# Performance work log

Hardware: AMD Instinct MI355X
Metric: run time of the kernel (lower is better)

Reference implementation:

```python
import jax, jax.numpy as jnp
import numpy as np
from jax.ops import segment_sum

N_NODES = 50000
N_EDGES = 800000
D_IN, D_HID, D_OUT = 128, 128, 64


def setup_inputs() -> dict:
    key = jax.random.key(0)
    ks = jax.random.split(key, 7)
    return {
        "src": jax.random.randint(ks[0], (N_EDGES,), 0, N_NODES, dtype=jnp.int32),
        "dst": jax.random.randint(ks[1], (N_EDGES,), 0, N_NODES, dtype=jnp.int32),
        "x": jax.random.normal(ks[2], (N_NODES, D_IN), dtype=jnp.float32),
        "W1": jax.random.normal(ks[3], (D_IN, D_HID), dtype=jnp.float32) * (1.0 / np.sqrt(D_IN)),
        "b1": jnp.zeros((D_HID,), dtype=jnp.float32),
        "W2": jax.random.normal(ks[4], (D_HID, D_OUT), dtype=jnp.float32) * (1.0 / np.sqrt(D_HID)),
        "b2": jnp.zeros((D_OUT,), dtype=jnp.float32),
    }


def _gcn_layer(src, dst, x, W, b, inv_sqrt_out, inv_sqrt_in):
    # DGL GraphConv, norm='both': h = D_in^{-1/2} A D_out^{-1/2} (x W) + b
    h = (x * inv_sqrt_out[:, None]) @ W          # transform first (in >= out)
    msg = h[src]                                  # gather source messages [E, d]
    agg = segment_sum(msg, dst, num_segments=x.shape[0])
    return agg * inv_sqrt_in[:, None] + b


def reference(src, dst, x, W1, b1, W2, b2):
    n = x.shape[0]
    ones = jnp.ones((src.shape[0],), dtype=x.dtype)
    deg_out = jnp.clip(segment_sum(ones, src, num_segments=n), 1.0)
    deg_in = jnp.clip(segment_sum(ones, dst, num_segments=n), 1.0)
    inv_sqrt_out = jax.lax.rsqrt(deg_out)
    inv_sqrt_in = jax.lax.rsqrt(deg_in)
    h = _gcn_layer(src, dst, x, W1, b1, inv_sqrt_out, inv_sqrt_in)
    h = jax.nn.relu(h)
    h = _gcn_layer(src, dst, h, W2, b2, inv_sqrt_out, inv_sqrt_in)
    return h
```

## Files before the change

kernel.cpp:

```cpp
#include <hip/hip_runtime.h>
#include <hip/hip_fp16.h>

#define D_IN  128
#define D_HID 128
#define D_OUT 64
#define NBMAX 512
#define CHUNK 2048
#define FCACHE 3072

typedef __attribute__((ext_vector_type(8))) short bf16x8;
typedef __attribute__((ext_vector_type(4))) float f32x4;

__device__ __forceinline__ unsigned short f2bf_rne(float f) {
    unsigned int u = __float_as_uint(f);
    return (unsigned short)((u + 0x7FFFu + ((u >> 16) & 1u)) >> 16);
}

__launch_bounds__(256)
__global__ void k_prep(const float* __restrict__ W1, const float* __restrict__ W2,
                       unsigned short* __restrict__ W1h, unsigned short* __restrict__ W1l,
                       unsigned short* __restrict__ W2h, unsigned short* __restrict__ W2l,
                       int* __restrict__ cntD, int* __restrict__ cntS, int NB) {
    const int b = blockIdx.x, t = threadIdx.x;
    if (b < 64) {
        const int i = b * 256 + t;
        const int k = i >> 7, j = i & 127;
        const float v = W1[i];
        const unsigned short hb = f2bf_rne(v);
        const float hf = __uint_as_float((unsigned int)hb << 16);
        W1h[j * 128 + k] = hb;
        W1l[j * 128 + k] = f2bf_rne(v - hf);
    } else if (b < 96) {
        const int i = (b - 64) * 256 + t;
        const int k = i >> 6, j = i & 63;
        const float v = W2[i];
        const unsigned short hb = f2bf_rne(v);
        const float hf = __uint_as_float((unsigned int)hb << 16);
        W2h[j * 128 + k] = hb;
        W2l[j * 128 + k] = f2bf_rne(v - hf);
    } else {
        for (int i = t; i < NB; i += 256) { cntD[i] = 0; cntS[i] = 0; }
    }
}

struct BucketS {
    int lc[512], ls[512];
    int baD[512], baS[512];
    int gbD[512], gbS[512];
    int ssum[256];
    unsigned int  ldsD[CHUNK];
    int           gposD[CHUNK];
    unsigned char ldsS[CHUNK];
    int           gposS[CHUNK];
};
struct GemmS {
    short Ah[32][136];
    short Al[32][136];
};
union SMem { BucketS b; GemmS g; };

__device__ __forceinline__ void bucket_body(
        BucketS& sm, int bx,
        const int* __restrict__ src, const int* __restrict__ dst,
        int E, int NB, int cap,
        int* __restrict__ cntD, int* __restrict__ cntS,
        unsigned int* __restrict__ storeD, unsigned char* __restrict__ storeS) {
    const int t = threadIdx.x;
    const int e0 = bx * CHUNK;
    const int e1 = min(e0 + CHUNK, E);
    const int n  = e1 - e0;

    int sv[8], dv[8];
#pragma unroll
    for (int u = 0; u < 8; ++u) {
        const int i = e0 + u * 256 + t;
        if (i < e1) { sv[u] = src[i]; dv[u] = dst[i]; }
        else        { sv[u] = -1;     dv[u] = -1; }
    }

    sm.lc[t] = 0; sm.lc[t + 256] = 0; sm.ls[t] = 0; sm.ls[t + 256] = 0;
    __syncthreads();
#pragma unroll
    for (int u = 0; u < 8; ++u) {
        if (sv[u] >= 0) {
            atomicAdd(&sm.lc[dv[u] >> 7], 1);
            atomicAdd(&sm.ls[sv[u] >> 7], 1);
        }
    }
    __syncthreads();

    const int c0 = sm.lc[2 * t], c1 = sm.lc[2 * t + 1];
    const int s0 = sm.ls[2 * t], s1 = sm.ls[2 * t + 1];
    {
        const int pc = c0 + c1;
        sm.ssum[t] = pc; __syncthreads();
        int inc = pc;
        for (int off = 1; off < 256; off <<= 1) {
            const int o = (t >= off) ? sm.ssum[t - off] : 0;
            __syncthreads();
            inc += o; sm.ssum[t] = inc;
            __syncthreads();
        }
        const int ex = inc - pc;
        sm.baD[2 * t] = ex; sm.baD[2 * t + 1] = ex + c0;
    }
    {
        const int ps = s0 + s1;
        sm.ssum[t] = ps; __syncthreads();
        int inc = ps;
        for (int off = 1; off < 256; off <<= 1) {
            const int o = (t >= off) ? sm.ssum[t - off] : 0;
            __syncthreads();
            inc += o; sm.ssum[t] = inc;
            __syncthreads();
        }
        const int ex = inc - ps;
        sm.baS[2 * t] = ex; sm.baS[2 * t + 1] = ex + s0;
    }
    __syncthreads();

    for (int i = t; i < NB; i += 256) {
        const int c = sm.lc[i];
        sm.gbD[i] = i * cap + (c ? atomicAdd(&cntD[i], c) : 0);
        const int s = sm.ls[i];
        sm.gbS[i] = i * cap + (s ? atomicAdd(&cntS[i], s) : 0);
    }
    __syncthreads();
    sm.lc[t] = 0; sm.lc[t + 256] = 0; sm.ls[t] = 0; sm.ls[t + 256] = 0;
    __syncthreads();

#pragma unroll
    for (int u = 0; u < 8; ++u) {
        if (sv[u] >= 0) {
            const int s = sv[u], d = dv[u];
            const int bd = d >> 7;
            const int lp = atomicAdd(&sm.lc[bd], 1);
            const int p  = sm.baD[bd] + lp;
            sm.ldsD[p]  = (unsigned int)s | ((unsigned int)(d & 127) << 16);
            sm.gposD[p] = sm.gbD[bd] + lp;
            const int bs = s >> 7;
            const int lq = atomicAdd(&sm.ls[bs], 1);
            const int q  = sm.baS[bs] + lq;
            sm.ldsS[q]  = (unsigned char)(s & 127);
            sm.gposS[q] = sm.gbS[bs] + lq;
        }
    }
    __syncthreads();

    for (int p = t; p < n; p += 256) {
        storeD[sm.gposD[p]] = sm.ldsD[p];
        storeS[sm.gposS[p]] = sm.ldsS[p];
    }
}

__device__ __forceinline__ void gemm1_body(
        GemmS& sm, int bx,
        const float* __restrict__ X,
        const unsigned short* __restrict__ Wth, const unsigned short* __restrict__ Wtl,
        __half* __restrict__ Y, int N) {
    const int t = threadIdx.x;
    const int row0 = bx * 32;

#pragma unroll
    for (int p = 0; p < 4; ++p) {
        const int idx = p * 256 + t;
        const int r   = idx >> 5;
        const int c4  = (idx & 31) << 2;
        const int gr  = row0 + r;
        float4 v = make_float4(0.f, 0.f, 0.f, 0.f);
        if (gr < N) v = *(const float4*)(X + (long long)gr * 128 + c4);
        const float f[4] = {v.x, v.y, v.z, v.w};
        short hh[4], ll[4];
#pragma unroll
        for (int i = 0; i < 4; ++i) {
            const unsigned short hb = f2bf_rne(f[i]);
            const float hf = __uint_as_float(((unsigned int)hb) << 16);
            hh[i] = (short)hb;
            ll[i] = (short)f2bf_rne(f[i] - hf);
        }
        *(short4*)&sm.Ah[r][c4] = make_short4(hh[0], hh[1], hh[2], hh[3]);
        *(short4*)&sm.Al[r][c4] = make_short4(ll[0], ll[1], ll[2], ll[3]);
    }
    __syncthreads();

    constexpr int NT = 4;
    const int w    = t >> 6;
    const int lane = t & 63;
    const int rg = w & 1, cg = w >> 1;
    const int lrow = lane & 15;
    const int lk   = (lane >> 4) << 3;
    const int colbase = cg * (16 * NT);

    f32x4 acc[NT];
#pragma unroll
    for (int n = 0; n < NT; ++n) acc[n] = (f32x4){0.f, 0.f, 0.f, 0.f};

#pragma unroll
    for (int ks = 0; ks < 4; ++ks) {
        const int k = ks * 32 + lk;
        const bf16x8 ah = *(const bf16x8*)&sm.Ah[rg * 16 + lrow][k];
        const bf16x8 al = *(const bf16x8*)&sm.Al[rg * 16 + lrow][k];
#pragma unroll
        for (int n = 0; n < NT; ++n) {
            const int col = colbase + n * 16 + lrow;
            const bf16x8 bh = *(const bf16x8*)(Wth + (size_t)col * 128 + k);
            const bf16x8 bl = *(const bf16x8*)(Wtl + (size_t)col * 128 + k);
            acc[n] = __builtin_amdgcn_mfma_f32_16x16x32_bf16(ah, bh, acc[n], 0, 0, 0);
            acc[n] = __builtin_amdgcn_mfma_f32_16x16x32_bf16(ah, bl, acc[n], 0, 0, 0);
            acc[n] = __builtin_amdgcn_mfma_f32_16x16x32_bf16(al, bh, acc[n], 0, 0, 0);
        }
    }

#pragma unroll
    for (int n = 0; n < NT; ++n) {
#pragma unroll
        for (int i = 0; i < 4; ++i) {
            const int r = row0 + rg * 16 + ((lane >> 4) << 2) + i;
            if (r < N)
                Y[(long long)r * D_HID + colbase + n * 16 + lrow] = __float2half(acc[n][i]);
        }
    }
}

__launch_bounds__(256)
__global__ void k_bucket_gemm(const int* __restrict__ src, const int* __restrict__ dst,
                              int E, int NB, int cap,
                              int* __restrict__ cntD, int* __restrict__ cntS,
                              unsigned int* __restrict__ storeD, unsigned char* __restrict__ storeS,
                              const float* __restrict__ X,
                              const unsigned short* __restrict__ Wth,
                              const unsigned short* __restrict__ Wtl,
                              __half* __restrict__ Y, int N, int nbBlk) {
    __shared__ SMem sm;
    const int bx = (int)blockIdx.x;
    if (bx < nbBlk)
        bucket_body(sm.b, bx, src, dst, E, NB, cap, cntD, cntS, storeD, storeS);
    else
        gemm1_body(sm.g, bx - nbBlk, X, Wth, Wtl, Y, N);
}

__launch_bounds__(256)
__global__ void k_fin(const unsigned int* __restrict__ storeD, const unsigned char* __restrict__ storeS,
                      const int* __restrict__ cntD, const int* __restrict__ cntS,
                      int cap, int N, int NB, int E,
                      int* __restrict__ rowptr, float* __restrict__ inv_in,
                      float* __restrict__ inv_out, unsigned short* __restrict__ csr_src) {
    __shared__ int fh[128];
    __shared__ int sc[128];
    __shared__ int cur[128];
    __shared__ int red[256];
    __shared__ unsigned int ecache[FCACHE];
    const int b = blockIdx.x, t = threadIdx.x;
    const long long sb = (long long)b * cap;

    int partial = 0;
    for (int i = t; i < b; i += 256) partial += cntD[i];
    red[t] = partial;
    __syncthreads();
    for (int off = 128; off > 0; off >>= 1) {
        if (t < off) red[t] += red[t + off];
        __syncthreads();
    }
    const int base = red[0];

    const int cnt = cntD[b];
    const bool cached = (cnt <= FCACHE);
    if (cached) {
        for (int i = t; i < cnt; i += 256) ecache[i] = storeD[sb + i];
    }

    if (t < 128) fh[t] = 0;
    __syncthreads();
    for (int i = t; i < cnt; i += 256) {
        const unsigned int e = cached ? ecache[i] : storeD[sb + i];
        atomicAdd(&fh[e >> 16], 1);
    }
    __syncthreads();
    if (t < 128) sc[t] = fh[t];
    __syncthreads();
    int inc = (t < 128) ? sc[t] : 0;
    for (int off = 1; off < 128; off <<= 1) {
        int o = (t >= off && t < 128) ? sc[t - off] : 0;
        __syncthreads();
        if (t < 128) { inc += o; sc[t] = inc; }
        __syncthreads();
    }
    if (t < 128) {
        const int excl = inc - fh[t];
        cur[t] = excl;
        const int node = (b << 7) + t;
        if (node < N) {
            rowptr[node] = base + excl;
            inv_in[node] = rsqrtf((float)max(fh[t], 1));
        }
    }
    if (b == NB - 1 && t == 128) rowptr[N] = E;
    __syncthreads();
    for (int i = t; i < cnt; i += 256) {
        const unsigned int e = cached ? ecache[i] : storeD[sb + i];
        const int pos = atomicAdd(&cur[e >> 16], 1);
        csr_src[base + pos] = (unsigned short)(e & 0xFFFFu);
    }

    __syncthreads();
    if (t < 128) fh[t] = 0;
    __syncthreads();
    const int cnts = cntS[b];
    for (int i = t; i < cnts; i += 256) atomicAdd(&fh[storeS[sb + i]], 1);
    __syncthreads();
    if (t < 128) {
        const int node = (b << 7) + t;
        if (node < N) inv_out[node] = rsqrtf((float)max(fh[t], 1));
    }
}

template<int LDN>
__launch_bounds__(256)
__global__ void k_gemm_mfma(const __half* __restrict__ X,
                            const unsigned short* __restrict__ Wth,
                            const unsigned short* __restrict__ Wtl,
                            __half* __restrict__ Y, int N) {
    __shared__ short Ah[32][136], Al[32][136];

    const int t = threadIdx.x;
    const int row0 = blockIdx.x * 32;

#pragma unroll
    for (int p = 0; p < 2; ++p) {
        const int idx = p * 256 + t;
        const int r   = idx >> 4;
        const int c8  = (idx & 15) << 3;
        const int gr  = row0 + r;
        uint4 raw = make_uint4(0u, 0u, 0u, 0u);
        if (gr < N) raw = *(const uint4*)(X + (long long)gr * 128 + c8);
        const __half2* hp = (const __half2*)&raw;
        short hh[8], ll[8];
#pragma unroll
        for (int u = 0; u < 4; ++u) {
            const float2 f2 = __half22float2(hp[u]);
            const float f[2] = {f2.x, f2.y};
#pragma unroll
            for (int q = 0; q < 2; ++q) {
                const unsigned short hb = f2bf_rne(f[q]);
                const float hf = __uint_as_float(((unsigned int)hb) << 16);
                hh[2 * u + q] = (short)hb;
                ll[2 * u + q] = (short)f2bf_rne(f[q] - hf);
            }
        }
        *(short4*)&Ah[r][c8]     = make_short4(hh[0], hh[1], hh[2], hh[3]);
        *(short4*)&Ah[r][c8 + 4] = make_short4(hh[4], hh[5], hh[6], hh[7]);
        *(short4*)&Al[r][c8]     = make_short4(ll[0], ll[1], ll[2], ll[3]);
        *(short4*)&Al[r][c8 + 4] = make_short4(ll[4], ll[5], ll[6], ll[7]);
    }
    __syncthreads();

    constexpr int NT = LDN / 32;
    const int w    = t >> 6;
    const int lane = t & 63;
    const int rg = w & 1, cg = w >> 1;
    const int lrow = lane & 15;
    const int lk   = (lane >> 4) << 3;
    const int colbase = cg * (16 * NT);

    f32x4 acc[NT];
#pragma unroll
    for (int n = 0; n < NT; ++n) acc[n] = (f32x4){0.f, 0.f, 0.f, 0.f};

#pragma unroll
    for (int ks = 0; ks < 4; ++ks) {
        const int k = ks * 32 + lk;
        const bf16x8 ah = *(const bf16x8*)&Ah[rg * 16 + lrow][k];
        const bf16x8 al = *(const bf16x8*)&Al[rg * 16 + lrow][k];
#pragma unroll
        for (int n = 0; n < NT; ++n) {
            const int col = colbase + n * 16 + lrow;
            const bf16x8 bh = *(const bf16x8*)(Wth + (size_t)col * 128 + k);
            const bf16x8 bl = *(const bf16x8*)(Wtl + (size_t)col * 128 + k);
            acc[n] = __builtin_amdgcn_mfma_f32_16x16x32_bf16(ah, bh, acc[n], 0, 0, 0);
            acc[n] = __builtin_amdgcn_mfma_f32_16x16x32_bf16(ah, bl, acc[n], 0, 0, 0);
            acc[n] = __builtin_amdgcn_mfma_f32_16x16x32_bf16(al, bh, acc[n], 0, 0, 0);
        }
    }

#pragma unroll
    for (int n = 0; n < NT; ++n) {
#pragma unroll
        for (int i = 0; i < 4; ++i) {
            const int r = row0 + rg * 16 + ((lane >> 4) << 2) + i;
            if (r < N)
                Y[(long long)r * LDN + colbase + n * 16 + lrow] = __float2half(acc[n][i]);
        }
    }
}

template<int D, bool RELU, bool SRCSCALE, typename TO>
__launch_bounds__(256)
__global__ void k_gather(const int* __restrict__ rowptr, const unsigned short* __restrict__ csr_src,
                         const __half* __restrict__ Y, const float* __restrict__ inv_in,
                         const float* __restrict__ inv_out, const float* __restrict__ b,
                         TO* __restrict__ out, int N, const float* __restrict__ inv_src) {
    const int wid  = (int)((blockIdx.x * 256u + threadIdx.x) >> 6);
    const int lane = threadIdx.x & 63;
    if (wid >= N) return;

    const int start = rowptr[wid];
    const int end   = rowptr[wid + 1];

    constexpr int LPE = D / 8;
    constexpr int EPW = 64 / LPE;
    const int grp  = lane / LPE;
    const int colh = (lane % LPE) * 8;

    float a[8];
#pragma unroll
    for (int u = 0; u < 8; ++u) a[u] = 0.0f;

    auto accum = [&](uint4 raw, float io) {
        const __half2* h = (const __half2*)&raw;
#pragma unroll
        for (int u = 0; u < 4; ++u) {
            const float2 f = __half22float2(h[u]);
            if constexpr (SRCSCALE) {
                a[2 * u]     += f.x * io;
                a[2 * u + 1] += f.y * io;
            } else {
                a[2 * u]     += f.x;
                a[2 * u + 1] += f.y;
            }
        }
    };

    for (int k = start; k < end; k += 64) {
        const int idx = k + lane;
        const int sv  = (idx < end) ? (int)csr_src[idx] : 0;
        const int cnt = min(64, end - k);
        int j = 0;
        for (; j + 8 * EPW <= cnt; j += 8 * EPW) {
            int s[8];
#pragma unroll
            for (int u = 0; u < 8; ++u) s[u] = __shfl(sv, j + u * EPW + grp);
            uint4 r[8];
#pragma unroll
            for (int u = 0; u < 8; ++u) r[u] = *(const uint4*)(Y + (long long)s[u] * D + colh);
            float io[8];
            if constexpr (SRCSCALE) {
#pragma unroll
                for (int u = 0; u < 8; ++u) io[u] = inv_src[s[u]];
            }
#pragma unroll
            for (int u = 0; u < 8; ++u) accum(r[u], SRCSCALE ? io[u] : 0.0f);
        }
        for (; j + 4 * EPW <= cnt; j += 4 * EPW) {
            int s[4];
#pragma unroll
            for (int u = 0; u < 4; ++u) s[u] = __shfl(sv, j + u * EPW + grp);
            uint4 r[4];
#pragma unroll
            for (int u = 0; u < 4; ++u) r[u] = *(const uint4*)(Y + (long long)s[u] * D + colh);
            float io[4];
            if constexpr (SRCSCALE) {
#pragma unroll
                for (int u = 0; u < 4; ++u) io[u] = inv_src[s[u]];
            }
#pragma unroll
            for (int u = 0; u < 4; ++u) accum(r[u], SRCSCALE ? io[u] : 0.0f);
        }
        for (; j < cnt; j += EPW) {
            const int jj = j + grp;
            const int s  = __shfl(sv, jj);
            if (jj < cnt) {
                const uint4 r = *(const uint4*)(Y + (long long)s * D + colh);
                accum(r, SRCSCALE ? inv_src[s] : 0.0f);
            }
        }
    }

#pragma unroll
    for (int u = 0; u < 8; ++u) a[u] += __shfl_down(a[u], 32);
#pragma unroll
    for (int u = 0; u < 8; ++u) a[u] += __shfl_down(a[u], 16);
    if (EPW == 8) {
#pragma unroll
        for (int u = 0; u < 8; ++u) a[u] += __shfl_down(a[u], 8);
    }

    if (lane < LPE) {
        const float ii = inv_in[wid];
        const float io = RELU ? inv_out[wid] : 0.0f;
        const float4 b0 = *(const float4*)(b + colh);
        const float4 b1 = *(const float4*)(b + colh + 4);
        float r[8];
        r[0] = a[0] * ii + b0.x; r[1] = a[1] * ii + b0.y;
        r[2] = a[2] * ii + b0.z; r[3] = a[3] * ii + b0.w;
        r[4] = a[4] * ii + b1.x; r[5] = a[5] * ii + b1.y;
        r[6] = a[6] * ii + b1.z; r[7] = a[7] * ii + b1.w;
        if (RELU) {
#pragma unroll
            for (int u = 0; u < 8; ++u) r[u] = fmaxf(r[u], 0.0f) * io;
        }
        if constexpr (sizeof(TO) == 2) {
            __half2 h0 = __float22half2_rn(make_float2(r[0], r[1]));
            __half2 h1 = __float22half2_rn(make_float2(r[2], r[3]));
            __half2 h2 = __float22half2_rn(make_float2(r[4], r[5]));
            __half2 h3 = __float22half2_rn(make_float2(r[6], r[7]));
            uint4 pk;
            pk.x = *(unsigned int*)&h0; pk.y = *(unsigned int*)&h1;
            pk.z = *(unsigned int*)&h2; pk.w = *(unsigned int*)&h3;
            *(uint4*)((__half*)out + (long long)wid * D + colh) = pk;
        } else {
            float* o = (float*)out + (long long)wid * D + colh;
            *(float4*)(o)     = make_float4(r[0], r[1], r[2], r[3]);
            *(float4*)(o + 4) = make_float4(r[4], r[5], r[6], r[7]);
        }
    }
}

extern "C" void kernel_launch(void* const* d_in, const int* in_sizes, int n_in,
                              void* d_out, int out_size, void* d_ws, size_t ws_size,
                              hipStream_t stream) {
    const int*   src = (const int*)d_in[0];
    const int*   dst = (const int*)d_in[1];
    const float* x   = (const float*)d_in[2];
    const float* W1  = (const float*)d_in[3];
    const float* b1  = (const float*)d_in[4];
    const float* W2  = (const float*)d_in[5];
    const float* b2  = (const float*)d_in[6];
    float* out = (float*)d_out;

    const int E  = in_sizes[0];
    const int N  = in_sizes[2] / D_IN;
    const int NB = (N + 127) >> 7;
    const int mean = E / NB;
    const int cap  = mean + mean / 4 + 128;

    char* ws = (char*)d_ws;
    size_t off = 0;
    auto alloc = [&](size_t bytes) -> void* {
        void* p = ws + off;
        off += (bytes + 255) & ~(size_t)255;
        return p;
    };
    float*          inv_out = (float*)alloc((size_t)N * 4);
    float*          inv_in  = (float*)alloc((size_t)N * 4);
    int*            rowptr  = (int*)alloc((size_t)(N + 1) * 4);
    int*            cntD    = (int*)alloc((size_t)NB * 4);
    int*            cntS    = (int*)alloc((size_t)NB * 4);
    unsigned int*   storeD  = (unsigned int*)alloc((size_t)NB * cap * 4);
    unsigned char*  storeS  = (unsigned char*)alloc((size_t)NB * cap);
    unsigned short* csr_src = (unsigned short*)alloc((size_t)E * 2);
    unsigned short* W1h     = (unsigned short*)alloc(128 * 128 * 2);
    unsigned short* W1l     = (unsigned short*)alloc(128 * 128 * 2);
    unsigned short* W2h     = (unsigned short*)alloc(64 * 128 * 2);
    unsigned short* W2l     = (unsigned short*)alloc(64 * 128 * 2);
    __half*         Y1      = (__half*)alloc((size_t)N * D_HID * 2);
    __half*         H       = (__half*)alloc((size_t)N * D_HID * 2);
    __half*         Y2      = (__half*)alloc((size_t)N * D_OUT * 2);
    (void)ws_size; (void)n_in; (void)out_size;

    const int nbBlk   = (E + CHUNK - 1) / CHUNK;
    const int gemmBlk = (N + 31) / 32;

    k_prep<<<97, 256, 0, stream>>>(W1, W2, W1h, W1l, W2h, W2l, cntD, cntS, NB);
    k_bucket_gemm<<<nbBlk + gemmBlk, 256, 0, stream>>>(src, dst, E, NB, cap, cntD, cntS,
                                                       storeD, storeS, x, W1h, W1l, Y1, N, nbBlk);
    k_fin<<<NB, 256, 0, stream>>>(storeD, storeS, cntD, cntS, cap, N, NB, E,
                                  rowptr, inv_in, inv_out, csr_src);

    k_gather<D_HID, true, true, __half><<<(N + 3) / 4, 256, 0, stream>>>(
        rowptr, csr_src, Y1, inv_in, inv_out, b1, H, N, inv_out);

    k_gemm_mfma<D_OUT><<<(N + 31) / 32, 256, 0, stream>>>(H, W2h, W2l, Y2, N);
    k_gather<D_OUT, false, false, float><<<(N + 3) / 4, 256, 0, stream>>>(
        rowptr, csr_src, Y2, inv_in, nullptr, b2, out, N, nullptr);
}
```

Measured before the change: 134.1 us.

## Fuse layer-1 gather with layer-2 GEMM and use wave-shuffle scan in bucketing

Merges the first-layer neighbour aggregation (with ReLU and scaling) into the second-layer MFMA GEMM kernel. Each block now gathers 32 rows into shared memory as split bf16 and multiplies them straight away, so the fp16 intermediate H no longer goes through global memory and one launch disappears. The block-wide Hillis-Steele scan in the bucketing step becomes a wave-level shuffle scan plus a small cross-wave sum, which removes many barriers. In exchange, the fused gather runs with far fewer blocks, 8 rows per wave processed serially, and a shallower unroll, which reduces memory-level parallelism in the gather.

After: 141.3 us. 5.4% more time.

```diff
diff --git a/kernel.cpp b/kernel.cpp
--- a/kernel.cpp
+++ b/kernel.cpp
@@ -47,7 +47,7 @@
     int lc[512], ls[512];
     int baD[512], baS[512];
     int gbD[512], gbS[512];
-    int ssum[256];
+    int wsumD[4], wsumS[4];
     unsigned int  ldsD[CHUNK];
     int           gposD[CHUNK];
     unsigned char ldsS[CHUNK];
@@ -91,32 +91,26 @@
 
     const int c0 = sm.lc[2 * t], c1 = sm.lc[2 * t + 1];
     const int s0 = sm.ls[2 * t], s1 = sm.ls[2 * t + 1];
-    {
-        const int pc = c0 + c1;
-        sm.ssum[t] = pc; __syncthreads();
-        int inc = pc;
-        for (int off = 1; off < 256; off <<= 1) {
-            const int o = (t >= off) ? sm.ssum[t - off] : 0;
-            __syncthreads();
-            inc += o; sm.ssum[t] = inc;
-            __syncthreads();
-        }
-        const int ex = inc - pc;
-        sm.baD[2 * t] = ex; sm.baD[2 * t + 1] = ex + c0;
-    }
-    {
-        const int ps = s0 + s1;
-        sm.ssum[t] = ps; __syncthreads();
-        int inc = ps;
-        for (int off = 1; off < 256; off <<= 1) {
-            const int o = (t >= off) ? sm.ssum[t - off] : 0;
-            __syncthreads();
-            inc += o; sm.ssum[t] = inc;
-            __syncthreads();
-        }
-        const int ex = inc - ps;
-        sm.baS[2 * t] = ex; sm.baS[2 * t + 1] = ex + s0;
-    }
+    const int pc = c0 + c1, ps = s0 + s1;
+    const int wl = t & 63, wv = t >> 6;
+    int incD = pc, incS = ps;
+#pragma unroll
+    for (int off = 1; off < 64; off <<= 1) {
+        const int oD = __shfl_up(incD, off);
+        const int oS = __shfl_up(incS, off);
+        if (wl >= off) { incD += oD; incS += oS; }
+    }
+    if (wl == 63) { sm.wsumD[wv] = incD; sm.wsumS[wv] = incS; }
+    __syncthreads();
+    int baseD = 0, baseS = 0;
+#pragma unroll
+    for (int ww = 0; ww < 4; ++ww) {
+        if (ww < wv) { baseD += sm.wsumD[ww]; baseS += sm.wsumS[ww]; }
+    }
+    const int exD = baseD + incD - pc;
+    const int exS = baseS + incS - ps;
+    sm.baD[2 * t] = exD; sm.baD[2 * t + 1] = exD + c0;
+    sm.baS[2 * t] = exS; sm.baS[2 * t + 1] = exS + s0;
     __syncthreads();
 
     for (int i = t; i < NB; i += 256) {
@@ -314,53 +308,119 @@
     }
 }
 
-template<int LDN>
 __launch_bounds__(256)
-__global__ void k_gemm_mfma(const __half* __restrict__ X,
-                            const unsigned short* __restrict__ Wth,
-                            const unsigned short* __restrict__ Wtl,
-                            __half* __restrict__ Y, int N) {
+__global__ void k_gather_gemm2(const int* __restrict__ rowptr, const unsigned short* __restrict__ csr_src,
+                               const __half* __restrict__ Y1, const float* __restrict__ inv_in,
+                               const float* __restrict__ inv_out, const float* __restrict__ b1,
+                               const unsigned short* __restrict__ W2h, const unsigned short* __restrict__ W2l,
+                               __half* __restrict__ Y2, int N) {
     __shared__ short Ah[32][136], Al[32][136];
-
     const int t = threadIdx.x;
+    const int w = t >> 6, lane = t & 63;
     const int row0 = blockIdx.x * 32;
-
-#pragma unroll
-    for (int p = 0; p < 2; ++p) {
-        const int idx = p * 256 + t;
-        const int r   = idx >> 4;
-        const int c8  = (idx & 15) << 3;
-        const int gr  = row0 + r;
-        uint4 raw = make_uint4(0u, 0u, 0u, 0u);
-        if (gr < N) raw = *(const uint4*)(X + (long long)gr * 128 + c8);
-        const __half2* hp = (const __half2*)&raw;
-        short hh[8], ll[8];
-#pragma unroll
-        for (int u = 0; u < 4; ++u) {
-            const float2 f2 = __half22float2(hp[u]);
-            const float f[2] = {f2.x, f2.y};
-#pragma unroll
-            for (int q = 0; q < 2; ++q) {
-                const unsigned short hb = f2bf_rne(f[q]);
+    const int grp  = lane >> 4;
+    const int colh = (lane & 15) * 8;
+
+    for (int i = 0; i < 8; ++i) {
+        const int noderow = w * 8 + i;
+        const int wid = row0 + noderow;
+
+        float a[8];
+#pragma unroll
+        for (int u = 0; u < 8; ++u) a[u] = 0.0f;
+
+        if (wid < N) {
+            const int start = rowptr[wid];
+            const int end   = rowptr[wid + 1];
+            for (int k = start; k < end; k += 64) {
+                const int idx = k + lane;
+                const int svv = (idx < end) ? (int)csr_src[idx] : 0;
+                const int cnt = min(64, end - k);
+                int j = 0;
+                for (; j + 16 <= cnt; j += 16) {
+                    int s[4];
+#pragma unroll
+                    for (int u = 0; u < 4; ++u) s[u] = __shfl(svv, j + u * 4 + grp);
+                    uint4 r[4];
+#pragma unroll
+                    for (int u = 0; u < 4; ++u) r[u] = *(const uint4*)(Y1 + (long long)s[u] * 128 + colh);
+                    float io[4];
+#pragma unroll
+                    for (int u = 0; u < 4; ++u) io[u] = inv_out[s[u]];
+#pragma unroll
+                    for (int u = 0; u < 4; ++u) {
+                        const __half2* h = (const __half2*)&r[u];
+#pragma unroll
+                        for (int q = 0; q < 4; ++q) {
+                            const float2 f = __half22float2(h[q]);
+                            a[2 * q]     += f.x * io[u];
+                            a[2 * q + 1] += f.y * io[u];
+                        }
+                    }
+                }
+                for (; j < cnt; j += 4) {
+                    const int jj = j + grp;
+                    const int s  = __shfl(svv, jj);
+                    if (jj < cnt) {
+                        const uint4 r = *(const uint4*)(Y1 + (long long)s * 128 + colh);
+                        const float io = inv_out[s];
+                        const __half2* h = (const __half2*)&r;
+#pragma unroll
+                        for (int q = 0; q < 4; ++q) {
+                            const float2 f = __half22float2(h[q]);
+                            a[2 * q]     += f.x * io;
+                            a[2 * q + 1] += f.y * io;
+                        }
+                    }
+                }
+            }
+        }
+
+#pragma unroll
+        for (int u = 0; u < 8; ++u) a[u] += __shfl_down(a[u], 32);
+#pragma unroll
+        for (int u = 0; u < 8; ++u) a[u] += __shfl_down(a[u], 16);
+
+        if (lane < 16) {
+            float r[8];
+            if (wid < N) {
+                const float ii = inv_in[wid];
+                const float io = inv_out[wid];
+                const float4 b0v = *(const float4*)(b1 + colh);
+                const float4 b1v = *(const float4*)(b1 + colh + 4);
+                r[0] = fmaxf(a[0] * ii + b0v.x, 0.f) * io;
+                r[1] = fmaxf(a[1] * ii + b0v.y, 0.f) * io;
+                r[2] = fmaxf(a[2] * ii + b0v.z, 0.f) * io;
+                r[3] = fmaxf(a[3] * ii + b0v.w, 0.f) * io;
+                r[4] = fmaxf(a[4] * ii + b1v.x, 0.f) * io;
+                r[5] = fmaxf(a[5] * ii + b1v.y, 0.f) * io;
+                r[6] = fmaxf(a[6] * ii + b1v.z, 0.f) * io;
+                r[7] = fmaxf(a[7] * ii + b1v.w, 0.f) * io;
+            } else {
+#pragma unroll
+                for (int u = 0; u < 8; ++u) r[u] = 0.0f;
+            }
+            short hh[8], ll[8];
+#pragma unroll
+            for (int u = 0; u < 8; ++u) {
+                const unsigned short hb = f2bf_rne(r[u]);
                 const float hf = __uint_as_float(((unsigned int)hb) << 16);
-                hh[2 * u + q] = (short)hb;
-                ll[2 * u + q] = (short)f2bf_rne(f[q] - hf);
+                hh[u] = (short)hb;
+                ll[u] = (short)f2bf_rne(r[u] - hf);
             }
-        }
-        *(short4*)&Ah[r][c8]     = make_short4(hh[0], hh[1], hh[2], hh[3]);
-        *(short4*)&Ah[r][c8 + 4] = make_short4(hh[4], hh[5], hh[6], hh[7]);
-        *(short4*)&Al[r][c8]     = make_short4(ll[0], ll[1], ll[2], ll[3]);
-        *(short4*)&Al[r][c8 + 4] = make_short4(ll[4], ll[5], ll[6], ll[7]);
-    }
-    __syncthreads();
-
-    constexpr int NT = LDN / 32;
-    const int w    = t >> 6;
-    const int lane = t & 63;
+            *(short4*)&Ah[noderow][colh]     = make_short4(hh[0], hh[1], hh[2], hh[3]);
+            *(short4*)&Ah[noderow][colh + 4] = make_short4(hh[4], hh[5], hh[6], hh[7]);
+            *(short4*)&Al[noderow][colh]     = make_short4(ll[0], ll[1], ll[2], ll[3]);
+            *(short4*)&Al[noderow][colh + 4] = make_short4(ll[4], ll[5], ll[6], ll[7]);
+        }
+    }
+    __syncthreads();
+
+    constexpr int NT = 2;
     const int rg = w & 1, cg = w >> 1;
     const int lrow = lane & 15;
     const int lk   = (lane >> 4) << 3;
-    const int colbase = cg * (16 * NT);
+    const int colbase = cg * 32;
 
     f32x4 acc[NT];
 #pragma unroll
@@ -374,8 +434,8 @@
 #pragma unroll
         for (int n = 0; n < NT; ++n) {
             const int col = colbase + n * 16 + lrow;
-            const bf16x8 bh = *(const bf16x8*)(Wth + (size_t)col * 128 + k);
-            const bf16x8 bl = *(const bf16x8*)(Wtl + (size_t)col * 128 + k);
+            const bf16x8 bh = *(const bf16x8*)(W2h + (size_t)col * 128 + k);
+            const bf16x8 bl = *(const bf16x8*)(W2l + (size_t)col * 128 + k);
             acc[n] = __builtin_amdgcn_mfma_f32_16x16x32_bf16(ah, bh, acc[n], 0, 0, 0);
             acc[n] = __builtin_amdgcn_mfma_f32_16x16x32_bf16(ah, bl, acc[n], 0, 0, 0);
             acc[n] = __builtin_amdgcn_mfma_f32_16x16x32_bf16(al, bh, acc[n], 0, 0, 0);
@@ -388,17 +448,16 @@
         for (int i = 0; i < 4; ++i) {
             const int r = row0 + rg * 16 + ((lane >> 4) << 2) + i;
             if (r < N)
-                Y[(long long)r * LDN + colbase + n * 16 + lrow] = __float2half(acc[n][i]);
-        }
-    }
-}
-
-template<int D, bool RELU, bool SRCSCALE, typename TO>
+                Y2[(long long)r * D_OUT + colbase + n * 16 + lrow] = __float2half(acc[n][i]);
+        }
+    }
+}
+
+template<int D>
 __launch_bounds__(256)
 __global__ void k_gather(const int* __restrict__ rowptr, const unsigned short* __restrict__ csr_src,
                          const __half* __restrict__ Y, const float* __restrict__ inv_in,
-                         const float* __restrict__ inv_out, const float* __restrict__ b,
-                         TO* __restrict__ out, int N, const float* __restrict__ inv_src) {
+                         const float* __restrict__ b, float* __restrict__ out, int N) {
     const int wid  = (int)((blockIdx.x * 256u + threadIdx.x) >> 6);
     const int lane = threadIdx.x & 63;
     if (wid >= N) return;
@@ -415,18 +474,13 @@
 #pragma unroll
     for (int u = 0; u < 8; ++u) a[u] = 0.0f;
 
-    auto accum = [&](uint4 raw, float io) {
+    auto accum = [&](uint4 raw) {
         const __half2* h = (const __half2*)&raw;
 #pragma unroll
         for (int u = 0; u < 4; ++u) {
             const float2 f = __half22float2(h[u]);
-            if constexpr (SRCSCALE) {
-                a[2 * u]     += f.x * io;
-                a[2 * u + 1] += f.y * io;
-            } else {
-                a[2 * u]     += f.x;
-                a[2 * u + 1] += f.y;
-            }
+            a[2 * u]     += f.x;
+            a[2 * u + 1] += f.y;
         }
     };
 
@@ -442,13 +496,8 @@
             uint4 r[8];
 #pragma unroll
             for (int u = 0; u < 8; ++u) r[u] = *(const uint4*)(Y + (long long)s[u] * D + colh);
-            float io[8];
-            if constexpr (SRCSCALE) {
-#pragma unroll
-                for (int u = 0; u < 8; ++u) io[u] = inv_src[s[u]];
-            }
-#pragma unroll
-            for (int u = 0; u < 8; ++u) accum(r[u], SRCSCALE ? io[u] : 0.0f);
+#pragma unroll
+            for (int u = 0; u < 8; ++u) accum(r[u]);
         }
         for (; j + 4 * EPW <= cnt; j += 4 * EPW) {
             int s[4];
@@ -457,20 +506,15 @@
             uint4 r[4];
 #pragma unroll
             for (int u = 0; u < 4; ++u) r[u] = *(const uint4*)(Y + (long long)s[u] * D + colh);
-            float io[4];
-            if constexpr (SRCSCALE) {
-#pragma unroll
-                for (int u = 0; u < 4; ++u) io[u] = inv_src[s[u]];
-            }
-#pragma unroll
-            for (int u = 0; u < 4; ++u) accum(r[u], SRCSCALE ? io[u] : 0.0f);
+#pragma unroll
+            for (int u = 0; u < 4; ++u) accum(r[u]);
         }
         for (; j < cnt; j += EPW) {
             const int jj = j + grp;
             const int s  = __shfl(sv, jj);
             if (jj < cnt) {
                 const uint4 r = *(const uint4*)(Y + (long long)s * D + colh);
-                accum(r, SRCSCALE ? inv_src[s] : 0.0f);
+                accum(r);
             }
         }
     }
@@ -479,39 +523,18 @@
     for (int u = 0; u < 8; ++u) a[u] += __shfl_down(a[u], 32);
 #pragma unroll
     for (int u = 0; u < 8; ++u) a[u] += __shfl_down(a[u], 16);
-    if (EPW == 8) {
-#pragma unroll
-        for (int u = 0; u < 8; ++u) a[u] += __shfl_down(a[u], 8);
-    }
+#pragma unroll
+    for (int u = 0; u < 8; ++u) a[u] += __shfl_down(a[u], 8);
 
     if (lane < LPE) {
         const float ii = inv_in[wid];
-        const float io = RELU ? inv_out[wid] : 0.0f;
         const float4 b0 = *(const float4*)(b + colh);
         const float4 b1 = *(const float4*)(b + colh + 4);
-        float r[8];
-        r[0] = a[0] * ii + b0.x; r[1] = a[1] * ii + b0.y;
-        r[2] = a[2] * ii + b0.z; r[3] = a[3] * ii + b0.w;
-        r[4] = a[4] * ii + b1.x; r[5] = a[5] * ii + b1.y;
-        r[6] = a[6] * ii + b1.z; r[7] = a[7] * ii + b1.w;
-        if (RELU) {
-#pragma unroll
-            for (int u = 0; u < 8; ++u) r[u] = fmaxf(r[u], 0.0f) * io;
-        }
-        if constexpr (sizeof(TO) == 2) {
-            __half2 h0 = __float22half2_rn(make_float2(r[0], r[1]));
-            __half2 h1 = __float22half2_rn(make_float2(r[2], r[3]));
-            __half2 h2 = __float22half2_rn(make_float2(r[4], r[5]));
-            __half2 h3 = __float22half2_rn(make_float2(r[6], r[7]));
-            uint4 pk;
-            pk.x = *(unsigned int*)&h0; pk.y = *(unsigned int*)&h1;
-            pk.z = *(unsigned int*)&h2; pk.w = *(unsigned int*)&h3;
-            *(uint4*)((__half*)out + (long long)wid * D + colh) = pk;
-        } else {
-            float* o = (float*)out + (long long)wid * D + colh;
-            *(float4*)(o)     = make_float4(r[0], r[1], r[2], r[3]);
-            *(float4*)(o + 4) = make_float4(r[4], r[5], r[6], r[7]);
-        }
+        float* o = out + (long long)wid * D + colh;
+        *(float4*)(o)     = make_float4(a[0] * ii + b0.x, a[1] * ii + b0.y,
+                                        a[2] * ii + b0.z, a[3] * ii + b0.w);
+        *(float4*)(o + 4) = make_float4(a[4] * ii + b1.x, a[5] * ii + b1.y,
+                                        a[6] * ii + b1.z, a[7] * ii + b1.w);
     }
 }
 
@@ -553,7 +576,6 @@
     unsigned short* W2h     = (unsigned short*)alloc(64 * 128 * 2);
     unsigned short* W2l     = (unsigned short*)alloc(64 * 128 * 2);
     __half*         Y1      = (__half*)alloc((size_t)N * D_HID * 2);
-    __half*         H       = (__half*)alloc((size_t)N * D_HID * 2);
     __half*         Y2      = (__half*)alloc((size_t)N * D_OUT * 2);
     (void)ws_size; (void)n_in; (void)out_size;
 
@@ -566,10 +588,8 @@
     k_fin<<<NB, 256, 0, stream>>>(storeD, storeS, cntD, cntS, cap, N, NB, E,
                                   rowptr, inv_in, inv_out, csr_src);
 
-    k_gather<D_HID, true, true, __half><<<(N + 3) / 4, 256, 0, stream>>>(
-        rowptr, csr_src, Y1, inv_in, inv_out, b1, H, N, inv_out);
-
-    k_gemm_mfma<D_OUT><<<(N + 31) / 32, 256, 0, stream>>>(H, W2h, W2l, Y2, N);
-    k_gather<D_OUT, false, false, float><<<(N + 3) / 4, 256, 0, stream>>>(
-        rowptr, csr_src, Y2, inv_in, nullptr, b2, out, N, nullptr);
-}
+    k_gather_gemm2<<<gemmBlk, 256, 0, stream>>>(rowptr, csr_src, Y1, inv_in, inv_out, b1,
+                                                W2h, W2l, Y2, N);
+
+    k_gather<D_OUT><<<(N + 3) / 4, 256, 0, stream>>>(rowptr, csr_src, Y2, inv_in, b2, out, N);
+}
```
